# Performance work log

Hardware: AMD Instinct MI355X
Metric: run time of the kernel (lower is better)

Reference implementation:

```python
import jax, jax.numpy as jnp
import numpy as np

V, E, H, L, B = 32004, 512, 512, 128, 64  # vocab(+4), emb, hidden, seq_len, batch


def setup_inputs() -> dict:
    key = jax.random.key(0)
    ks = jax.random.split(key, 8)
    emb = jax.random.normal(ks[0], (V, E), jnp.float32) * 0.02
    emb = emb.at[0].set(0.0)  # padding_idx = PAD = 0
    Wx_f = jax.random.normal(ks[1], (E, 3 * H), jnp.float32) * 0.05
    Wh_f = jax.random.normal(ks[2], (H, 3 * H), jnp.float32) * 0.05
    b_f = jnp.zeros((3 * H,), jnp.float32)
    Wx_b = jax.random.normal(ks[3], (E, 3 * H), jnp.float32) * 0.05
    Wh_b = jax.random.normal(ks[4], (H, 3 * H), jnp.float32) * 0.05
    b_b = jnp.zeros((3 * H,), jnp.float32)
    xs = jax.random.randint(ks[5], (L, B), 0, V)
    xs_mask = jnp.ones((L, B), jnp.float32)
    return {"xs": xs, "xs_mask": xs_mask, "emb": emb,
            "Wx_f": Wx_f, "Wh_f": Wh_f, "b_f": b_f,
            "Wx_b": Wx_b, "Wh_b": Wh_b, "b_b": b_b}


def _gru_scan(xs_e, mask, Wx, Wh, b, reverse):
    # Precompute all input-to-gate projections in one big GEMM: [L,B,3H]
    xw = jnp.einsum('lbe,eg->lbg', xs_e, Wx) + b

    def step(h, inp):
        xw_t, m = inp                       # [B,3H], [B]
        hw = h @ Wh                         # [B,3H]
        xz, xr, xh = jnp.split(xw_t, 3, -1)
        hz, hr, hh = jnp.split(hw, 3, -1)
        z = jax.nn.sigmoid(xz + hz)
        r = jax.nn.sigmoid(xr + hr)
        h_tilde = jnp.tanh(xh + r * hh)
        h_new = (1.0 - z) * h + z * h_tilde
        m = m[:, None]
        h_new = m * h_new + (1.0 - m) * h   # masked timesteps keep previous state
        return h_new, h_new

    h0 = jnp.zeros((xs_e.shape[1], Wh.shape[0]), xs_e.dtype)
    _, hs = jax.lax.scan(step, h0, (xw, mask), reverse=reverse)
    return hs  # [L,B,H], time-ordered (reverse=True already yields original order)


def reference(xs, xs_mask, emb, Wx_f, Wh_f, b_f, Wx_b, Wh_b, b_b):
    xs_e = emb[xs]                                   # [L,B,E]
    right = _gru_scan(xs_e, xs_mask, Wx_f, Wh_f, b_f, reverse=False)
    left = _gru_scan(xs_e, xs_mask, Wx_b, Wh_b, b_b, reverse=True)
    r1 = jnp.concatenate([right, left], axis=-1)      # [L,B,2H]
    r2 = left[0]                                      # final backward state (after t=0)
    return r1, r2
```

## Files before the change

kernel.cpp:

```cpp
#include <hip/hip_runtime.h>
#include <stdint.h>

typedef _Float16 f16;
typedef _Float16 f16x8 __attribute__((ext_vector_type(8)));
typedef float    f32x4 __attribute__((ext_vector_type(4)));
typedef unsigned long long u64;

#define L_    128
#define B_    64
#define E_    512
#define H_    512
#define G3    1536
#define NCOL  3072

__device__ __forceinline__ float sigm_(float x){ return 1.0f/(1.0f + __expf(-x)); }
__device__ __forceinline__ float tanh_(float x){ return 1.0f - 2.0f/(__expf(2.0f*x) + 1.0f); }

__global__ __launch_bounds__(256) void k_embed(const int* __restrict__ xs,
                                               const float* __restrict__ emb,
                                               f16* __restrict__ Xe,
                                               uint4* __restrict__ flags4){
  if (blockIdx.x == 0){
    flags4[threadIdx.x]       = make_uint4(0,0,0,0);
    flags4[256 + threadIdx.x] = make_uint4(0,0,0,0);
  }
  int row = blockIdx.x*2 + (threadIdx.x >> 7);
  int c   = (threadIdx.x & 127) * 4;
  int idx = xs[row];
  float4 v = *(const float4*)(emb + (size_t)idx*E_ + c);
  union { f16 h[4]; uint2 u; } p;
  p.h[0] = (f16)v.x; p.h[1] = (f16)v.y; p.h[2] = (f16)v.z; p.h[3] = (f16)v.w;
  *(uint2*)(Xe + (size_t)row*E_ + c) = p.u;
}

__global__ __launch_bounds__(256) void k_transpose(const float* __restrict__ Wx_f, const float* __restrict__ Wx_b,
                                                   const float* __restrict__ Wh_f, const float* __restrict__ Wh_b,
                                                   f16* __restrict__ WxT, f16* __restrict__ WhT){
  int mat = blockIdx.z;
  const float* src = mat==0 ? Wx_f : mat==1 ? Wx_b : mat==2 ? Wh_f : Wh_b;
  f16* dst = (mat < 2) ? (WxT + (size_t)mat*G3*E_) : (WhT + (size_t)(mat-2)*G3*H_);
  int n0 = blockIdx.x*64, k0 = blockIdx.y*64;
  __shared__ f16 tile[64][65];
  int tid = threadIdx.x;
  for (int i=0;i<16;i++){
    int r = i*4 + (tid>>6);
    int c = tid & 63;
    tile[r][c] = (f16)src[(size_t)(k0+r)*G3 + n0 + c];
  }
  __syncthreads();
  for (int i=0;i<16;i++){
    int n = i*4 + (tid>>6);
    int k = tid & 63;
    dst[(size_t)(n0+n)*512 + k0 + k] = tile[k][n];
  }
}

__global__ __launch_bounds__(256) void k_gemm(const f16* __restrict__ Xe, const f16* __restrict__ WxT,
                                              const float* __restrict__ bf, const float* __restrict__ bb,
                                              f16* __restrict__ xw2){
  __shared__ __align__(16) f16 sA[128*32];
  __shared__ __align__(16) f16 sB[128*32];
  const int tid = threadIdx.x;
  const int l = tid & 63, w = tid >> 6;
  const int wr = w >> 1, wc = w & 1;
  const int m0 = blockIdx.y*128, n0 = blockIdx.x*128;
  const int rl = l & 15, sg = l >> 4;
  f32x4 acc[4][4] = {};
  for (int kk=0; kk<16; ++kk){
    __syncthreads();
    for (int i=0;i<2;i++){
      int c = i*256 + tid; int row = c>>2, s = c&3;
      int sw = s ^ ((row>>1)&3);
      *(uint4*)&sA[row*32 + sw*8] = *(const uint4*)(Xe  + (size_t)(m0+row)*512 + kk*32 + s*8);
      *(uint4*)&sB[row*32 + sw*8] = *(const uint4*)(WxT + (size_t)(n0+row)*512 + kk*32 + s*8);
    }
    __syncthreads();
    f16x8 a[4], b[4];
    for (int mi=0;mi<4;mi++){ int m=(wr*4+mi)*16+rl; a[mi] = *(const f16x8*)&sA[m*32 + ((sg^((m>>1)&3))*8)]; }
    for (int nj=0;nj<4;nj++){ int n=(wc*4+nj)*16+rl; b[nj] = *(const f16x8*)&sB[n*32 + ((sg^((n>>1)&3))*8)]; }
    for (int mi=0;mi<4;mi++)
      for (int nj=0;nj<4;nj++)
        acc[mi][nj] = __builtin_amdgcn_mfma_f32_16x16x32_f16(a[mi], b[nj], acc[mi][nj], 0,0,0);
  }
  for (int nj=0;nj<4;nj++){
    int n = n0 + (wc*4+nj)*16 + rl;
    float bias = (n < G3) ? bf[n] : bb[n-G3];
    for (int mi=0;mi<4;mi++){
      int sub = (wr*4+mi)*16 + sg*4;
      int t   = (m0 + sub) >> 6;
      int b0  = sub & 63;
      union { f16 h[4]; uint2 u; } p;
      for (int r=0;r<4;r++) p.h[r] = (f16)(acc[mi][nj][r] + bias);
      *(uint2*)(xw2 + ((size_t)t*NCOL + n)*B_ + b0) = p.u;
    }
  }
}

__global__ __launch_bounds__(128, 1) void k_scan(const f16* __restrict__ xw2, const f16* __restrict__ WhT,
                                                 f16* __restrict__ hbuf, const float* __restrict__ mask,
                                                 float* __restrict__ out, unsigned* __restrict__ flags){
  const int dir = blockIdx.x >> 6;
  const int m   = (blockIdx.x >> 4) & 3;
  const int n   = blockIdx.x & 15;
  const int gidx = dir*4 + m;
  __shared__ __align__(16) f16 sX[2*16*16];
  const int tid = threadIdx.x, l = tid & 63, wv = tid >> 6;
  const int fl = l & 15, sg = l >> 4;
  const int fbase = n*32 + wv*16;
  f16x8 pz[16], pr[16], ph[16];
  {
    const f16* wb = WhT + (size_t)dir*G3*512;
    #pragma unroll
    for (int kk=0;kk<16;kk++){
      int ko = kk*32 + sg*8;
      pz[kk] = *(const f16x8*)(wb + (size_t)(       fbase + fl)*512 + ko);
      pr[kk] = *(const f16x8*)(wb + (size_t)( 512 + fbase + fl)*512 + ko);
      ph[kk] = *(const f16x8*)(wb + (size_t)(1024 + fbase + fl)*512 + ko);
    }
  }
  #pragma unroll
  for (int kk=0;kk<16;kk++){
    asm volatile("" : "+v"(pz[kk]));
    asm volatile("" : "+v"(pr[kk]));
    asm volatile("" : "+v"(ph[kk]));
  }
  float hstate[4] = {0.f,0.f,0.f,0.f};
  float* out2 = out + (size_t)L_*B_*1024;
  const int mb = m*16 + sg*4;
  unsigned* myflag = flags + (size_t)(n*8 + gidx)*16;
  const unsigned* pollp = flags + (size_t)((l&15)*8 + gidx)*16;
  f16* const sXw = &sX[wv*256];
  const int prow = l >> 2, pf = (l & 3)*4;

  for (int ti=0; ti<128; ++ti){
    const int t = dir ? (127 - ti) : ti;
    size_t xb = ((size_t)t*NCOL + dir*G3 + fbase + fl)*B_ + mb;
    union { uint2 u; f16 h[4]; } xzv, xrv, xhv;
    xzv.u = *(const uint2*)(xw2 + xb);
    xrv.u = *(const uint2*)(xw2 + xb + (size_t)512*B_);
    xhv.u = *(const uint2*)(xw2 + xb + (size_t)1024*B_);
    float4 mv4 = *(const float4*)(mask + t*B_ + mb);
    f32x4 az = {0,0,0,0}, ar = {0,0,0,0}, ah = {0,0,0,0};
    if (ti){
      unsigned tgt = (unsigned)ti;
      while (true){
        unsigned f = __hip_atomic_load(pollp, __ATOMIC_RELAXED, __HIP_MEMORY_SCOPE_AGENT);
        if (__all((int)(f >= tgt))) break;
      }
      const u64* hq = (const u64*)(hbuf + ((size_t)gidx*2 + (ti&1))*(16*512)) + (size_t)fl*128;
      u64 q[32];
      #pragma unroll
      for (int kk=0;kk<16;kk++){
        int j = kk*8 + sg*2;
        q[2*kk  ] = __hip_atomic_load(hq + j,     __ATOMIC_RELAXED, __HIP_MEMORY_SCOPE_AGENT);
        q[2*kk+1] = __hip_atomic_load(hq + j + 1, __ATOMIC_RELAXED, __HIP_MEMORY_SCOPE_AGENT);
      }
      #pragma unroll
      for (int kk=0;kk<16;kk++){
        union { u64 d[2]; f16x8 h; } a;
        a.d[0] = q[2*kk]; a.d[1] = q[2*kk+1];
        az = __builtin_amdgcn_mfma_f32_16x16x32_f16(a.h, pz[kk], az, 0,0,0);
        ar = __builtin_amdgcn_mfma_f32_16x16x32_f16(a.h, pr[kk], ar, 0,0,0);
        ah = __builtin_amdgcn_mfma_f32_16x16x32_f16(a.h, ph[kk], ah, 0,0,0);
      }
    }
    #pragma unroll
    for (int r=0;r<4;r++){
      float z  = sigm_((float)xzv.h[r] + az[r]);
      float rr = sigm_((float)xrv.h[r] + ar[r]);
      float ht = tanh_((float)xhv.h[r] + rr*ah[r]);
      float mv = (&mv4.x)[r];
      float hn = (1.0f - z)*hstate[r] + z*ht;
      hn = mv*hn + (1.0f - mv)*hstate[r];
      hstate[r] = hn;
    }
    if (ti < 127){
      #pragma unroll
      for (int r=0;r<4;r++) sXw[(sg*4 + r)*16 + fl] = (f16)hstate[r];
      asm volatile("s_waitcnt lgkmcnt(0)" ::: "memory");
      u64 v = *(const u64*)&sXw[prow*16 + pf];
      f16* hb = hbuf + ((size_t)gidx*2 + ((ti&1)^1))*(16*512);
      __hip_atomic_store((u64*)(hb + (size_t)prow*512 + n*32 + wv*16 + pf), v,
                         __ATOMIC_RELAXED, __HIP_MEMORY_SCOPE_AGENT);
      __syncthreads();
      if (tid == 0)
        __hip_atomic_store(myflag, (unsigned)(ti+1),
                           __ATOMIC_RELAXED, __HIP_MEMORY_SCOPE_AGENT);
    }
    #pragma unroll
    for (int r=0;r<4;r++)
      out[((size_t)(t*B_ + mb + r))*1024 + dir*512 + fbase + fl] = hstate[r];
    if (dir==1 && t==0){
      #pragma unroll
      for (int r=0;r<4;r++)
        out2[(size_t)(mb + r)*512 + fbase + fl] = hstate[r];
    }
  }
}

extern "C" void kernel_launch(void* const* d_in, const int* in_sizes, int n_in,
                              void* d_out, int out_size, void* d_ws, size_t ws_size,
                              hipStream_t stream){
  const int*   xs      = (const int*)  d_in[0];
  const float* xs_mask = (const float*)d_in[1];
  const float* emb     = (const float*)d_in[2];
  const float* Wx_f    = (const float*)d_in[3];
  const float* Wh_f    = (const float*)d_in[4];
  const float* b_f     = (const float*)d_in[5];
  const float* Wx_b    = (const float*)d_in[6];
  const float* Wh_b    = (const float*)d_in[7];
  const float* b_b     = (const float*)d_in[8];

  char* w = (char*)d_ws;
  f16*      Xe    = (f16*)(w);
  f16*      WxT   = (f16*)(w + 8388608);
  f16*      WhT   = (f16*)(w + 11534336);
  f16*      xw2   = (f16*)(w + 14680064);
  f16*      hbuf  = (f16*)(w + 65011712);
  unsigned* flags = (unsigned*)(w + 65273856);
  float*    out   = (float*)d_out;

  k_embed    <<<dim3(4096),    dim3(256), 0, stream>>>(xs, emb, Xe, (uint4*)flags);
  k_transpose<<<dim3(24,8,4),  dim3(256), 0, stream>>>(Wx_f, Wx_b, Wh_f, Wh_b, WxT, WhT);
  k_gemm     <<<dim3(24,64),   dim3(256), 0, stream>>>(Xe, WxT, b_f, b_b, xw2);
  k_scan     <<<dim3(128),     dim3(128), 0, stream>>>(xw2, WhT, hbuf, xs_mask, out, flags);
}
```

Baseline: 613.4 us.

## Replace shared h buffer with per-block sentinel inboxes pushed by producers

Each scan block now has its own 4-deep ring of inbox slots. Producers broadcast their new hidden-state slice to all 16 blocks in the group, so consumers read from a private buffer and detect arrival through an all-ones sentinel value rather than relying only on the flag poll. The inbox region reuses the Xe workspace and is pre-filled with sentinels by a new fill kernel. Per-wave flags replace the block-wide __syncthreads before the flag store. This aims to cut cross-block handoff latency per timestep, at the cost of 16x the store traffic and an extra kernel launch. It also relies on a genuine fp16 payload never equalling the sentinel.

```diff
diff --git a/kernel.cpp b/kernel.cpp
--- a/kernel.cpp
+++ b/kernel.cpp
@@ -12,6 +12,7 @@
 #define H_    512
 #define G3    1536
 #define NCOL  3072
+#define IBSZ  16384
 
 __device__ __forceinline__ float sigm_(float x){ return 1.0f/(1.0f + __expf(-x)); }
 __device__ __forceinline__ float tanh_(float x){ return 1.0f - 2.0f/(__expf(2.0f*x) + 1.0f); }
@@ -96,8 +97,12 @@
   }
 }
 
+__global__ __launch_bounds__(256) void k_fill(uint4* p){
+  p[(size_t)blockIdx.x*256 + threadIdx.x] = make_uint4(~0u,~0u,~0u,~0u);
+}
+
 __global__ __launch_bounds__(128, 1) void k_scan(const f16* __restrict__ xw2, const f16* __restrict__ WhT,
-                                                 f16* __restrict__ hbuf, const float* __restrict__ mask,
+                                                 char* __restrict__ inb, const float* __restrict__ mask,
                                                  float* __restrict__ out, unsigned* __restrict__ flags){
   const int dir = blockIdx.x >> 6;
   const int m   = (blockIdx.x >> 4) & 3;
@@ -127,13 +132,21 @@
   float hstate[4] = {0.f,0.f,0.f,0.f};
   float* out2 = out + (size_t)L_*B_*1024;
   const int mb = m*16 + sg*4;
-  unsigned* myflag = flags + (size_t)(n*8 + gidx)*16;
-  const unsigned* pollp = flags + (size_t)((l&15)*8 + gidx)*16;
+  unsigned* myflag = flags + ((size_t)(n*2 + wv)*8 + gidx)*8;
+  const unsigned* pollp = flags + ((size_t)(l & 31)*8 + gidx)*8;
   f16* const sXw = &sX[wv*256];
   const int prow = l >> 2, pf = (l & 3)*4;
+  char* const ginb = inb + (size_t)(gidx*16)*4*IBSZ;
+  char* const myinb = ginb + (size_t)n*4*IBSZ;
 
   for (int ti=0; ti<128; ++ti){
     const int t = dir ? (127 - ti) : ti;
+    if (ti >= 2){
+      u64* rb = (u64*)(myinb + (size_t)((ti-1)&3)*IBSZ);
+      #pragma unroll
+      for (int k2=0;k2<8;k2++)
+        __hip_atomic_store(rb + tid + 128*k2, ~0ull, __ATOMIC_RELAXED, __HIP_MEMORY_SCOPE_AGENT);
+    }
     size_t xb = ((size_t)t*NCOL + dir*G3 + fbase + fl)*B_ + mb;
     union { uint2 u; f16 h[4]; } xzv, xrv, xhv;
     xzv.u = *(const uint2*)(xw2 + xb);
@@ -147,14 +160,27 @@
         unsigned f = __hip_atomic_load(pollp, __ATOMIC_RELAXED, __HIP_MEMORY_SCOPE_AGENT);
         if (__all((int)(f >= tgt))) break;
       }
-      const u64* hq = (const u64*)(hbuf + ((size_t)gidx*2 + (ti&1))*(16*512)) + (size_t)fl*128;
+      const u64* ib = (const u64*)(myinb + (size_t)(ti&3)*IBSZ) + (size_t)fl*128;
       u64 q[32];
       #pragma unroll
       for (int kk=0;kk<16;kk++){
         int j = kk*8 + sg*2;
-        q[2*kk  ] = __hip_atomic_load(hq + j,     __ATOMIC_RELAXED, __HIP_MEMORY_SCOPE_AGENT);
-        q[2*kk+1] = __hip_atomic_load(hq + j + 1, __ATOMIC_RELAXED, __HIP_MEMORY_SCOPE_AGENT);
-      }
+        q[2*kk  ] = __hip_atomic_load(ib + j,     __ATOMIC_RELAXED, __HIP_MEMORY_SCOPE_AGENT);
+        q[2*kk+1] = __hip_atomic_load(ib + j + 1, __ATOMIC_RELAXED, __HIP_MEMORY_SCOPE_AGENT);
+      }
+      while (true){
+        int ok = 1;
+        #pragma unroll
+        for (int i=0;i<32;i++) ok &= (int)(q[i] != ~0ull);
+        if (__all(ok)) break;
+        #pragma unroll
+        for (int kk=0;kk<16;kk++){
+          int j = kk*8 + sg*2;
+          if (q[2*kk  ] == ~0ull) q[2*kk  ] = __hip_atomic_load(ib + j,     __ATOMIC_RELAXED, __HIP_MEMORY_SCOPE_AGENT);
+          if (q[2*kk+1] == ~0ull) q[2*kk+1] = __hip_atomic_load(ib + j + 1, __ATOMIC_RELAXED, __HIP_MEMORY_SCOPE_AGENT);
+        }
+      }
+      __syncthreads();
       #pragma unroll
       for (int kk=0;kk<16;kk++){
         union { u64 d[2]; f16x8 h; } a;
@@ -179,11 +205,16 @@
       for (int r=0;r<4;r++) sXw[(sg*4 + r)*16 + fl] = (f16)hstate[r];
       asm volatile("s_waitcnt lgkmcnt(0)" ::: "memory");
       u64 v = *(const u64*)&sXw[prow*16 + pf];
-      f16* hb = hbuf + ((size_t)gidx*2 + ((ti&1)^1))*(16*512);
-      __hip_atomic_store((u64*)(hb + (size_t)prow*512 + n*32 + wv*16 + pf), v,
-                         __ATOMIC_RELAXED, __HIP_MEMORY_SCOPE_AGENT);
-      __syncthreads();
-      if (tid == 0)
+      asm volatile("s_waitcnt vmcnt(0)" ::: "memory");
+      const size_t gofs = (size_t)prow*128 + ((fbase + pf) >> 2);
+      const size_t bofs = (size_t)((ti+1)&3)*IBSZ;
+      #pragma unroll
+      for (int c=0;c<16;c++){
+        int cc = (n + c) & 15;
+        u64* dst = (u64*)(ginb + (size_t)cc*4*IBSZ + bofs) + gofs;
+        __hip_atomic_store(dst, v, __ATOMIC_RELAXED, __HIP_MEMORY_SCOPE_AGENT);
+      }
+      if (l == 0)
         __hip_atomic_store(myflag, (unsigned)(ti+1),
                            __ATOMIC_RELAXED, __HIP_MEMORY_SCOPE_AGENT);
     }
@@ -213,15 +244,16 @@
 
   char* w = (char*)d_ws;
   f16*      Xe    = (f16*)(w);
+  char*     inbox = w;
   f16*      WxT   = (f16*)(w + 8388608);
   f16*      WhT   = (f16*)(w + 11534336);
   f16*      xw2   = (f16*)(w + 14680064);
-  f16*      hbuf  = (f16*)(w + 65011712);
   unsigned* flags = (unsigned*)(w + 65273856);
   float*    out   = (float*)d_out;
 
   k_embed    <<<dim3(4096),    dim3(256), 0, stream>>>(xs, emb, Xe, (uint4*)flags);
   k_transpose<<<dim3(24,8,4),  dim3(256), 0, stream>>>(Wx_f, Wx_b, Wh_f, Wh_b, WxT, WhT);
   k_gemm     <<<dim3(24,64),   dim3(256), 0, stream>>>(Xe, WxT, b_f, b_b, xw2);
-  k_scan     <<<dim3(128),     dim3(128), 0, stream>>>(xw2, WhT, hbuf, xs_mask, out, flags);
-}
+  k_fill     <<<dim3(2048),    dim3(256), 0, stream>>>((uint4*)inbox);
+  k_scan     <<<dim3(128),     dim3(128), 0, stream>>>(xw2, WhT, inbox, xs_mask, out, flags);
+}
```

Result: slower. 824.2 us (+34.4%).

## Interleave forward and backward GRU scans in each block, halving scan grid

Applied to the files above, without the earlier changes.

Each scan block now runs both directions, alternating a forward step and a backward step inside one time loop, so the scan grid drops from 128 to 64 blocks. Forward recurrent weights stay in registers, while the backward weights sit in an XOR-swizzled 96KB LDS buffer. The aim is to hide each direction's cross-block flag polling and hidden-state exchange latency behind the other direction's work. In exchange, each block does twice the serial work per step, backward weights are read from LDS every step, and half as many CUs are used.

```diff
diff --git a/kernel.cpp b/kernel.cpp
--- a/kernel.cpp
+++ b/kernel.cpp
@@ -99,17 +99,16 @@
 __global__ __launch_bounds__(128, 1) void k_scan(const f16* __restrict__ xw2, const f16* __restrict__ WhT,
                                                  f16* __restrict__ hbuf, const float* __restrict__ mask,
                                                  float* __restrict__ out, unsigned* __restrict__ flags){
-  const int dir = blockIdx.x >> 6;
-  const int m   = (blockIdx.x >> 4) & 3;
-  const int n   = blockIdx.x & 15;
-  const int gidx = dir*4 + m;
+  const int m = blockIdx.x >> 4;
+  const int n = blockIdx.x & 15;
+  __shared__ __align__(16) f16 sWb[96*512];
   __shared__ __align__(16) f16 sX[2*16*16];
   const int tid = threadIdx.x, l = tid & 63, wv = tid >> 6;
   const int fl = l & 15, sg = l >> 4;
   const int fbase = n*32 + wv*16;
   f16x8 pz[16], pr[16], ph[16];
   {
-    const f16* wb = WhT + (size_t)dir*G3*512;
+    const f16* wb = WhT;
     #pragma unroll
     for (int kk=0;kk<16;kk++){
       int ko = kk*32 + sg*8;
@@ -124,76 +123,160 @@
     asm volatile("" : "+v"(pr[kk]));
     asm volatile("" : "+v"(ph[kk]));
   }
-  float hstate[4] = {0.f,0.f,0.f,0.f};
+  {
+    const f16* base = WhT + (size_t)G3*512;
+    int cs = tid & 15;
+    for (int r = tid>>4; r < 96; r += 8){
+      int rowg = (r>>5)*512 + n*32 + (r&31);
+      const uint4* src = (const uint4*)(base + (size_t)rowg*512);
+      for (int j=0;j<4;j++){
+        int s = cs*4 + j;
+        *(uint4*)&sWb[r*512 + ((s^(r&7))*8)] = src[s];
+      }
+    }
+  }
+  __syncthreads();
+  float hf[4] = {0.f,0.f,0.f,0.f};
+  float hbk[4] = {0.f,0.f,0.f,0.f};
   float* out2 = out + (size_t)L_*B_*1024;
   const int mb = m*16 + sg*4;
-  unsigned* myflag = flags + (size_t)(n*8 + gidx)*16;
-  const unsigned* pollp = flags + (size_t)((l&15)*8 + gidx)*16;
+  unsigned* myflag_f = flags + (size_t)(n*8 + m)*16;
+  unsigned* myflag_b = flags + (size_t)(n*8 + 4 + m)*16;
+  const unsigned* pollp_f = flags + (size_t)((l&15)*8 + m)*16;
+  const unsigned* pollp_b = flags + (size_t)((l&15)*8 + 4 + m)*16;
   f16* const sXw = &sX[wv*256];
   const int prow = l >> 2, pf = (l & 3)*4;
 
   for (int ti=0; ti<128; ++ti){
-    const int t = dir ? (127 - ti) : ti;
-    size_t xb = ((size_t)t*NCOL + dir*G3 + fbase + fl)*B_ + mb;
-    union { uint2 u; f16 h[4]; } xzv, xrv, xhv;
-    xzv.u = *(const uint2*)(xw2 + xb);
-    xrv.u = *(const uint2*)(xw2 + xb + (size_t)512*B_);
-    xhv.u = *(const uint2*)(xw2 + xb + (size_t)1024*B_);
-    float4 mv4 = *(const float4*)(mask + t*B_ + mb);
-    f32x4 az = {0,0,0,0}, ar = {0,0,0,0}, ah = {0,0,0,0};
-    if (ti){
-      unsigned tgt = (unsigned)ti;
-      while (true){
-        unsigned f = __hip_atomic_load(pollp, __ATOMIC_RELAXED, __HIP_MEMORY_SCOPE_AGENT);
-        if (__all((int)(f >= tgt))) break;
-      }
-      const u64* hq = (const u64*)(hbuf + ((size_t)gidx*2 + (ti&1))*(16*512)) + (size_t)fl*128;
-      u64 q[32];
+    {
+      const int t = ti;
+      size_t xb = ((size_t)t*NCOL + fbase + fl)*B_ + mb;
+      union { uint2 u; f16 h[4]; } xzv, xrv, xhv;
+      xzv.u = *(const uint2*)(xw2 + xb);
+      xrv.u = *(const uint2*)(xw2 + xb + (size_t)512*B_);
+      xhv.u = *(const uint2*)(xw2 + xb + (size_t)1024*B_);
+      float4 mv4 = *(const float4*)(mask + t*B_ + mb);
+      f32x4 az = {0,0,0,0}, ar = {0,0,0,0}, ah = {0,0,0,0};
+      if (ti){
+        unsigned tgt = (unsigned)ti;
+        while (true){
+          unsigned f = __hip_atomic_load(pollp_f, __ATOMIC_RELAXED, __HIP_MEMORY_SCOPE_AGENT);
+          if (__all((int)(f >= tgt))) break;
+        }
+        const u64* hq = (const u64*)(hbuf + ((size_t)m*2 + (ti&1))*(16*512)) + (size_t)fl*128;
+        u64 q[32];
+        #pragma unroll
+        for (int kk=0;kk<16;kk++){
+          int j = kk*8 + sg*2;
+          q[2*kk  ] = __hip_atomic_load(hq + j,     __ATOMIC_RELAXED, __HIP_MEMORY_SCOPE_AGENT);
+          q[2*kk+1] = __hip_atomic_load(hq + j + 1, __ATOMIC_RELAXED, __HIP_MEMORY_SCOPE_AGENT);
+        }
+        #pragma unroll
+        for (int kk=0;kk<16;kk++){
+          union { u64 d[2]; f16x8 h; } a;
+          a.d[0] = q[2*kk]; a.d[1] = q[2*kk+1];
+          az = __builtin_amdgcn_mfma_f32_16x16x32_f16(a.h, pz[kk], az, 0,0,0);
+          ar = __builtin_amdgcn_mfma_f32_16x16x32_f16(a.h, pr[kk], ar, 0,0,0);
+          ah = __builtin_amdgcn_mfma_f32_16x16x32_f16(a.h, ph[kk], ah, 0,0,0);
+        }
+      }
       #pragma unroll
-      for (int kk=0;kk<16;kk++){
-        int j = kk*8 + sg*2;
-        q[2*kk  ] = __hip_atomic_load(hq + j,     __ATOMIC_RELAXED, __HIP_MEMORY_SCOPE_AGENT);
-        q[2*kk+1] = __hip_atomic_load(hq + j + 1, __ATOMIC_RELAXED, __HIP_MEMORY_SCOPE_AGENT);
-      }
-      #pragma unroll
-      for (int kk=0;kk<16;kk++){
-        union { u64 d[2]; f16x8 h; } a;
-        a.d[0] = q[2*kk]; a.d[1] = q[2*kk+1];
-        az = __builtin_amdgcn_mfma_f32_16x16x32_f16(a.h, pz[kk], az, 0,0,0);
-        ar = __builtin_amdgcn_mfma_f32_16x16x32_f16(a.h, pr[kk], ar, 0,0,0);
-        ah = __builtin_amdgcn_mfma_f32_16x16x32_f16(a.h, ph[kk], ah, 0,0,0);
-      }
-    }
-    #pragma unroll
-    for (int r=0;r<4;r++){
-      float z  = sigm_((float)xzv.h[r] + az[r]);
-      float rr = sigm_((float)xrv.h[r] + ar[r]);
-      float ht = tanh_((float)xhv.h[r] + rr*ah[r]);
-      float mv = (&mv4.x)[r];
-      float hn = (1.0f - z)*hstate[r] + z*ht;
-      hn = mv*hn + (1.0f - mv)*hstate[r];
-      hstate[r] = hn;
-    }
-    if (ti < 127){
-      #pragma unroll
-      for (int r=0;r<4;r++) sXw[(sg*4 + r)*16 + fl] = (f16)hstate[r];
-      asm volatile("s_waitcnt lgkmcnt(0)" ::: "memory");
-      u64 v = *(const u64*)&sXw[prow*16 + pf];
-      f16* hb = hbuf + ((size_t)gidx*2 + ((ti&1)^1))*(16*512);
-      __hip_atomic_store((u64*)(hb + (size_t)prow*512 + n*32 + wv*16 + pf), v,
-                         __ATOMIC_RELAXED, __HIP_MEMORY_SCOPE_AGENT);
-      __syncthreads();
-      if (tid == 0)
-        __hip_atomic_store(myflag, (unsigned)(ti+1),
+      for (int r=0;r<4;r++){
+        float z  = sigm_((float)xzv.h[r] + az[r]);
+        float rr = sigm_((float)xrv.h[r] + ar[r]);
+        float ht = tanh_((float)xhv.h[r] + rr*ah[r]);
+        float mv = (&mv4.x)[r];
+        float hn = (1.0f - z)*hf[r] + z*ht;
+        hn = mv*hn + (1.0f - mv)*hf[r];
+        hf[r] = hn;
+      }
+      if (ti < 127){
+        #pragma unroll
+        for (int r=0;r<4;r++) sXw[(sg*4 + r)*16 + fl] = (f16)hf[r];
+        asm volatile("s_waitcnt lgkmcnt(0)" ::: "memory");
+        u64 v = *(const u64*)&sXw[prow*16 + pf];
+        f16* hb = hbuf + ((size_t)m*2 + ((ti&1)^1))*(16*512);
+        __hip_atomic_store((u64*)(hb + (size_t)prow*512 + n*32 + wv*16 + pf), v,
                            __ATOMIC_RELAXED, __HIP_MEMORY_SCOPE_AGENT);
-    }
-    #pragma unroll
-    for (int r=0;r<4;r++)
-      out[((size_t)(t*B_ + mb + r))*1024 + dir*512 + fbase + fl] = hstate[r];
-    if (dir==1 && t==0){
+        __syncthreads();
+        if (tid == 0)
+          __hip_atomic_store(myflag_f, (unsigned)(ti+1),
+                             __ATOMIC_RELAXED, __HIP_MEMORY_SCOPE_AGENT);
+      }
       #pragma unroll
       for (int r=0;r<4;r++)
-        out2[(size_t)(mb + r)*512 + fbase + fl] = hstate[r];
+        out[((size_t)(t*B_ + mb + r))*1024 + fbase + fl] = hf[r];
+    }
+    {
+      const int t = 127 - ti;
+      size_t xb = ((size_t)t*NCOL + G3 + fbase + fl)*B_ + mb;
+      union { uint2 u; f16 h[4]; } xzv, xrv, xhv;
+      xzv.u = *(const uint2*)(xw2 + xb);
+      xrv.u = *(const uint2*)(xw2 + xb + (size_t)512*B_);
+      xhv.u = *(const uint2*)(xw2 + xb + (size_t)1024*B_);
+      float4 mv4 = *(const float4*)(mask + t*B_ + mb);
+      f32x4 az = {0,0,0,0}, ar = {0,0,0,0}, ah = {0,0,0,0};
+      if (ti){
+        unsigned tgt = (unsigned)ti;
+        while (true){
+          unsigned f = __hip_atomic_load(pollp_b, __ATOMIC_RELAXED, __HIP_MEMORY_SCOPE_AGENT);
+          if (__all((int)(f >= tgt))) break;
+        }
+        const u64* hq = (const u64*)(hbuf + ((size_t)(4+m)*2 + (ti&1))*(16*512)) + (size_t)fl*128;
+        u64 q[32];
+        #pragma unroll
+        for (int kk=0;kk<16;kk++){
+          int j = kk*8 + sg*2;
+          q[2*kk  ] = __hip_atomic_load(hq + j,     __ATOMIC_RELAXED, __HIP_MEMORY_SCOPE_AGENT);
+          q[2*kk+1] = __hip_atomic_load(hq + j + 1, __ATOMIC_RELAXED, __HIP_MEMORY_SCOPE_AGENT);
+        }
+        #pragma unroll
+        for (int kk=0;kk<16;kk++){
+          union { u64 d[2]; f16x8 h; } a;
+          a.d[0] = q[2*kk]; a.d[1] = q[2*kk+1];
+          int s = kk*4 + sg;
+          int r0 =      wv*16 + fl;
+          int r1 = 32 + wv*16 + fl;
+          int r2 = 64 + wv*16 + fl;
+          f16x8 b0 = *(const f16x8*)&sWb[r0*512 + ((s^(r0&7))*8)];
+          f16x8 b1 = *(const f16x8*)&sWb[r1*512 + ((s^(r1&7))*8)];
+          f16x8 b2 = *(const f16x8*)&sWb[r2*512 + ((s^(r2&7))*8)];
+          az = __builtin_amdgcn_mfma_f32_16x16x32_f16(a.h, b0, az, 0,0,0);
+          ar = __builtin_amdgcn_mfma_f32_16x16x32_f16(a.h, b1, ar, 0,0,0);
+          ah = __builtin_amdgcn_mfma_f32_16x16x32_f16(a.h, b2, ah, 0,0,0);
+        }
+      }
+      #pragma unroll
+      for (int r=0;r<4;r++){
+        float z  = sigm_((float)xzv.h[r] + az[r]);
+        float rr = sigm_((float)xrv.h[r] + ar[r]);
+        float ht = tanh_((float)xhv.h[r] + rr*ah[r]);
+        float mv = (&mv4.x)[r];
+        float hn = (1.0f - z)*hbk[r] + z*ht;
+        hn = mv*hn + (1.0f - mv)*hbk[r];
+        hbk[r] = hn;
+      }
+      if (ti < 127){
+        #pragma unroll
+        for (int r=0;r<4;r++) sXw[(sg*4 + r)*16 + fl] = (f16)hbk[r];
+        asm volatile("s_waitcnt lgkmcnt(0)" ::: "memory");
+        u64 v = *(const u64*)&sXw[prow*16 + pf];
+        f16* hb = hbuf + ((size_t)(4+m)*2 + ((ti&1)^1))*(16*512);
+        __hip_atomic_store((u64*)(hb + (size_t)prow*512 + n*32 + wv*16 + pf), v,
+                           __ATOMIC_RELAXED, __HIP_MEMORY_SCOPE_AGENT);
+        __syncthreads();
+        if (tid == 0)
+          __hip_atomic_store(myflag_b, (unsigned)(ti+1),
+                             __ATOMIC_RELAXED, __HIP_MEMORY_SCOPE_AGENT);
+      }
+      #pragma unroll
+      for (int r=0;r<4;r++)
+        out[((size_t)(t*B_ + mb + r))*1024 + 512 + fbase + fl] = hbk[r];
+      if (ti == 127){
+        #pragma unroll
+        for (int r=0;r<4;r++)
+          out2[(size_t)(mb + r)*512 + fbase + fl] = hbk[r];
+      }
     }
   }
 }
@@ -223,5 +306,5 @@
   k_embed    <<<dim3(4096),    dim3(256), 0, stream>>>(xs, emb, Xe, (uint4*)flags);
   k_transpose<<<dim3(24,8,4),  dim3(256), 0, stream>>>(Wx_f, Wx_b, Wh_f, Wh_b, WxT, WhT);
   k_gemm     <<<dim3(24,64),   dim3(256), 0, stream>>>(Xe, WxT, b_f, b_b, xw2);
-  k_scan     <<<dim3(128),     dim3(128), 0, stream>>>(xw2, WhT, hbuf, xs_mask, out, flags);
-}
+  k_scan     <<<dim3(64),      dim3(128), 0, stream>>>(xw2, WhT, hbuf, xs_mask, out, flags);
+}
```

Measured after the change: 1.106 ms. 1.8x slower.
